# Performance work log

Measured on AMD Instinct MI355X. Metric: run time of the kernel, lower is better.

Reference implementation:

```python
import jax, jax.numpy as jnp
from jax import lax
import numpy as np

T, B, D, H = 512, 256, 128, 256
SHIFT = 0.0


def setup_inputs() -> dict:
    key = jax.random.key(0)
    ks = jax.random.split(key, 11)
    s_in = 1.0 / np.sqrt(D + H)
    s_cl = 1.0 / np.sqrt(H)
    return {
        "inputs": jax.random.normal(ks[0], (T, B, D), dtype=jnp.float32),
        "Wf": jax.random.normal(ks[1], (H, D + H), dtype=jnp.float32) * s_in,
        "bf": jax.random.normal(ks[2], (H,), dtype=jnp.float32) * s_in,
        "Wi": jax.random.normal(ks[3], (H, D + H), dtype=jnp.float32) * s_in,
        "bi": jax.random.normal(ks[4], (H,), dtype=jnp.float32) * s_in,
        "Wg": jax.random.normal(ks[5], (H, D + H), dtype=jnp.float32) * s_in,
        "bg": jax.random.normal(ks[6], (H,), dtype=jnp.float32) * s_in,
        "Wo": jax.random.normal(ks[7], (H, D + H), dtype=jnp.float32) * s_in,
        "bo": jax.random.normal(ks[8], (H,), dtype=jnp.float32) * s_in,
        "Wc": jax.random.normal(ks[9], (1, H), dtype=jnp.float32) * s_cl,
        "bc": jax.random.normal(ks[10], (1,), dtype=jnp.float32) * s_cl,
    }


def reference(inputs, Wf, bf, Wi, bi, Wg, bg, Wo, bo, Wc, bc):
    # Fuse the four gate linears into one GEMM per step: [4H, D+H]
    W = jnp.concatenate([Wf, Wi, Wg, Wo], axis=0)
    b = jnp.concatenate([bf, bi, bg, bo], axis=0)
    h = W.shape[0] // 4
    batch = inputs.shape[1]

    def step(carry, x):
        hx, cx = carry
        combined = jnp.concatenate([x, hx], axis=1)      # [B, D+H]
        z = combined @ W.T + b                            # [B, 4H]
        f = jax.nn.sigmoid(z[:, 0 * h:1 * h])
        i = jax.nn.sigmoid(z[:, 1 * h:2 * h])
        g = jnp.tanh(z[:, 2 * h:3 * h])
        o = jax.nn.sigmoid(z[:, 3 * h:4 * h])
        cx = f * cx + i * g
        hx = o * jnp.tanh(cx)
        return (hx, cx), hx

    h0 = jnp.zeros((batch, h), dtype=inputs.dtype)
    c0 = jnp.zeros((batch, h), dtype=inputs.dtype)
    (hx, cx), hs = lax.scan(step, (h0, c0), inputs)       # hs: [T, B, H]

    logits = hs @ Wc.T + bc                               # [T, B, 1]
    probs = jax.nn.sigmoid(logits + SHIFT)
    return (jnp.concatenate([probs, 1.0 - probs], axis=-1), hx, cx)
```

## Files before the change

kernel.cpp:

```cpp
#include <hip/hip_runtime.h>
#include <hip/hip_bf16.h>


#define T_STEPS 512
#define BATCH   256
#define DIN     128
#define HID     256
#define KDIM    384
#define LDK     392
#define GRIDN   256
#define NPOLL   96

typedef __attribute__((ext_vector_type(8))) short short8;
typedef __attribute__((ext_vector_type(4))) short short4v;
typedef __attribute__((ext_vector_type(4))) float f32x4;

__device__ __forceinline__ unsigned short f2bf(float f) {
    unsigned u = __float_as_uint(f);
    unsigned r = (u + 0x7FFFu + ((u >> 16) & 1u)) >> 16;
    return (unsigned short)r;
}
__device__ __forceinline__ float bf2f(unsigned short s) {
    return __uint_as_float(((unsigned)s) << 16);
}
__device__ __forceinline__ float sigmoid_f(float x) {
    return 1.f / (1.f + __expf(-x));
}
__device__ __forceinline__ float tanh_f(float x) {
    float e = __expf(2.f * x);
    return 1.f - 2.f / (e + 1.f);
}
__device__ __forceinline__ void poll_load_sc0(const unsigned int* p, uint4& a,
                                              uint4& b, uint4& c, uint4& d) {
    asm volatile(
        "global_load_dwordx4 %0, %4, off sc0\n\t"
        "global_load_dwordx4 %1, %4, off offset:16 sc0\n\t"
        "global_load_dwordx4 %2, %4, off offset:32 sc0\n\t"
        "global_load_dwordx4 %3, %4, off offset:48 sc0\n\t"
        "s_waitcnt vmcnt(0)"
        : "=&v"(a), "=&v"(b), "=&v"(c), "=&v"(d) : "v"(p) : "memory");
}
__device__ __forceinline__ void poll_load_sc1(const unsigned int* p, uint4& a,
                                              uint4& b, uint4& c, uint4& d) {
    asm volatile(
        "global_load_dwordx4 %0, %4, off sc1\n\t"
        "global_load_dwordx4 %1, %4, off offset:16 sc1\n\t"
        "global_load_dwordx4 %2, %4, off offset:32 sc1\n\t"
        "global_load_dwordx4 %3, %4, off offset:48 sc1\n\t"
        "s_waitcnt vmcnt(0)"
        : "=&v"(a), "=&v"(b), "=&v"(c), "=&v"(d) : "v"(p) : "memory");
}
__device__ __forceinline__ void store_plain_u32(unsigned int* p, unsigned int v) {
    asm volatile("global_store_dword %0, %1, off" :: "v"(p), "v"(v) : "memory");
}
__device__ __forceinline__ void store_sc1_u32(unsigned int* p, unsigned int v) {
    asm volatile("global_store_dword %0, %1, off sc1" :: "v"(p), "v"(v) : "memory");
}
__device__ __forceinline__ unsigned pack2bf(unsigned lo, unsigned hi) {
    return (hi & 0xFFFF0000u) | (lo >> 16);
}
__device__ __forceinline__ bool tags_ok(const uint4& a, const uint4& b,
                                        const uint4& c, const uint4& d,
                                        unsigned tag) {
    return ((a.x ^ tag) & 0xFFFFu) == 0 && ((a.y ^ tag) & 0xFFFFu) == 0 &&
           ((a.z ^ tag) & 0xFFFFu) == 0 && ((a.w ^ tag) & 0xFFFFu) == 0 &&
           ((b.x ^ tag) & 0xFFFFu) == 0 && ((b.y ^ tag) & 0xFFFFu) == 0 &&
           ((b.z ^ tag) & 0xFFFFu) == 0 && ((b.w ^ tag) & 0xFFFFu) == 0 &&
           ((c.x ^ tag) & 0xFFFFu) == 0 && ((c.y ^ tag) & 0xFFFFu) == 0 &&
           ((c.z ^ tag) & 0xFFFFu) == 0 && ((c.w ^ tag) & 0xFFFFu) == 0 &&
           ((d.x ^ tag) & 0xFFFFu) == 0 && ((d.y ^ tag) & 0xFFFFu) == 0 &&
           ((d.z ^ tag) & 0xFFFFu) == 0 && ((d.w ^ tag) & 0xFFFFu) == 0;
}

__global__ __launch_bounds__(256) void pack_w(
    const float* __restrict__ Wf, const float* __restrict__ Wi,
    const float* __restrict__ Wg, const float* __restrict__ Wo,
    unsigned short* __restrict__ Wp) {
    int idx = blockIdx.x * 256 + threadIdx.x;
    int n = idx / KDIM;
    int k = idx - n * KDIM;
    int g = n >> 8, j = n & 255;
    const float* s = (g == 0) ? Wf : (g == 1) ? Wi : (g == 2) ? Wg : Wo;
    Wp[idx] = f2bf(s[j * KDIM + k]);
}

__global__ __launch_bounds__(256) void pack_b(
    const float* __restrict__ bf, const float* __restrict__ bi,
    const float* __restrict__ bg, const float* __restrict__ bo,
    float* __restrict__ bp) {
    int n = blockIdx.x * 256 + threadIdx.x;
    int g = n >> 8, j = n & 255;
    const float* s = (g == 0) ? bf : (g == 1) ? bi : (g == 2) ? bg : bo;
    bp[n] = s[j];
}

__global__ __launch_bounds__(256) void init_k(unsigned int* __restrict__ hxp) {
    int tid = blockIdx.x * 256 + threadIdx.x;
    hxp[tid] = 0u;
    hxp[65536 + tid] = 0u;
    hxp[131072 + tid] = 0u;
    hxp[196608 + tid] = 0u;
}

__global__ __launch_bounds__(256, 1) void lstm_persist(
    const float* __restrict__ X,
    const unsigned short* __restrict__ W,
    const float* __restrict__ bias,
    unsigned int* __restrict__ hxp,
    unsigned short* __restrict__ hist,
    float* __restrict__ out) {
    __shared__ __align__(16) unsigned short W_s[64 * LDK];
    __shared__ __align__(16) unsigned short comb_s[16 * LDK];
    __shared__ __align__(16) float z_s[4 * 272];
    __shared__ int fastok_s;

    const int tid = threadIdx.x;
    const int bg = blockIdx.x & 15, jg = blockIdx.x >> 4;
    const int b0 = bg * 16, j0 = jg * 16;
    const int wave = tid >> 6, lane = tid & 63;
    const int l16 = lane & 15, quad = lane >> 4;
    const int bi = tid >> 4, jj = tid & 15;
    const int b = b0 + bi, j = j0 + jj;

#pragma unroll
    for (int c = 0; c < 12; ++c) {
        int q = c * 256 + tid;
        int row = q / 48, c8 = q - row * 48;
        int g = row >> 4, jr = row & 15;
        short8 v = *(const short8*)(W + ((g * 256 + j0 + jr) * KDIM + c8 * 8));
        *(short8*)(&W_s[row * LDK + c8 * 8]) = v;
    }
    const float bs0 = bias[0 * HID + j];
    const float bs1 = bias[1 * HID + j];
    const float bs2 = bias[2 * HID + j];
    const float bs3 = bias[3 * HID + j];
    if (tid == 0) fastok_s = 1;

    float c_reg = 0.f;
    float h_final = 0.f;

    const unsigned short* arow = &comb_s[l16 * LDK + quad * 8];
    const unsigned short* brow = &W_s[(wave * 16 + l16) * LDK + quad * 8];
    const int hrow = tid >> 4, hc = tid & 15;
    const int xr0 = tid >> 5, xc4 = tid & 31, xr1 = (tid + 256) >> 5;

    const float* xb = X + b0 * DIN;
    float4 xv0 = *(const float4*)(xb + xr0 * DIN + xc4 * 4);
    float4 xv1 = *(const float4*)(xb + xr1 * DIN + xc4 * 4);

    __syncthreads();

    for (int k = 0; k < T_STEPS; ++k) {
        const unsigned tag = (unsigned)k;
        const unsigned int* fb =
            hxp + (k & 1) * 65536 + (b0 + hrow) * HID + hc * 16;
        const unsigned int* sb = fb + 131072;
        uint4 a, bq, cq, d;
        const int usefast = fastok_s;

        {
            short4v r;
            r.x = (short)f2bf(xv0.x); r.y = (short)f2bf(xv0.y);
            r.z = (short)f2bf(xv0.z); r.w = (short)f2bf(xv0.w);
            *(short4v*)(&comb_s[xr0 * LDK + xc4 * 4]) = r;
            r.x = (short)f2bf(xv1.x); r.y = (short)f2bf(xv1.y);
            r.z = (short)f2bf(xv1.z); r.w = (short)f2bf(xv1.w);
            *(short4v*)(&comb_s[xr1 * LDK + xc4 * 4]) = r;
        }

        if (usefast) {
            int tries = NPOLL;
            bool ok = false;
            for (;;) {
                poll_load_sc0(fb, a, bq, cq, d);
                if (tags_ok(a, bq, cq, d, tag)) { ok = true; break; }
                if (--tries == 0) break;
            }
            if (!ok) {
                fastok_s = 0;
                for (;;) {
                    poll_load_sc1(sb, a, bq, cq, d);
                    if (tags_ok(a, bq, cq, d, tag)) break;
                    __builtin_amdgcn_s_sleep(1);
                }
            }
        } else {
            for (;;) {
                poll_load_sc1(sb, a, bq, cq, d);
                if (tags_ok(a, bq, cq, d, tag)) break;
                __builtin_amdgcn_s_sleep(1);
            }
        }

        {
            uint4 p0, p1;
            p0.x = pack2bf(a.x, a.y);   p0.y = pack2bf(a.z, a.w);
            p0.z = pack2bf(bq.x, bq.y); p0.w = pack2bf(bq.z, bq.w);
            p1.x = pack2bf(cq.x, cq.y); p1.y = pack2bf(cq.z, cq.w);
            p1.z = pack2bf(d.x, d.y);   p1.w = pack2bf(d.z, d.w);
            *(uint4*)(&comb_s[hrow * LDK + DIN + hc * 16]) = p0;
            *(uint4*)(&comb_s[hrow * LDK + DIN + hc * 16 + 8]) = p1;
        }
        __syncthreads();

        f32x4 acc0 = {0.f, 0.f, 0.f, 0.f}, acc1 = {0.f, 0.f, 0.f, 0.f};
#pragma unroll
        for (int kt = 0; kt < 6; ++kt) {
            short8 a0 = *(const short8*)(arow + (2 * kt) * 32);
            short8 b0v = *(const short8*)(brow + (2 * kt) * 32);
            short8 a1 = *(const short8*)(arow + (2 * kt + 1) * 32);
            short8 b1v = *(const short8*)(brow + (2 * kt + 1) * 32);
            acc0 = __builtin_amdgcn_mfma_f32_16x16x32_bf16(a0, b0v, acc0, 0, 0, 0);
            acc1 = __builtin_amdgcn_mfma_f32_16x16x32_bf16(a1, b1v, acc1, 0, 0, 0);
        }
#pragma unroll
        for (int r = 0; r < 4; ++r)
            z_s[wave * 272 + (quad * 4 + r) * 17 + l16] = acc0[r] + acc1[r];
        __syncthreads();

        float zf = z_s[0 * 272 + bi * 17 + jj] + bs0;
        float zi = z_s[1 * 272 + bi * 17 + jj] + bs1;
        float zg = z_s[2 * 272 + bi * 17 + jj] + bs2;
        float zo = z_s[3 * 272 + bi * 17 + jj] + bs3;
        float fg = sigmoid_f(zf);
        float ig = sigmoid_f(zi);
        float gg = tanh_f(zg);
        float og = sigmoid_f(zo);
        c_reg = fg * c_reg + ig * gg;
        float hval = og * tanh_f(c_reg);
        unsigned short hb = f2bf(hval);
        unsigned int hword = ((unsigned)hb << 16) | (unsigned)(k + 1);
        unsigned int* fdst = hxp + ((k + 1) & 1) * 65536 + b * HID + j;
        store_plain_u32(fdst, hword);
        store_sc1_u32(fdst + 131072, hword);
        hist[(size_t)k * BATCH * HID + b * HID + j] = hb;
        if (k + 1 < T_STEPS) {
            const float* xn = X + (size_t)(k + 1) * BATCH * DIN + b0 * DIN;
            xv0 = *(const float4*)(xn + xr0 * DIN + xc4 * 4);
            xv1 = *(const float4*)(xn + xr1 * DIN + xc4 * 4);
        } else {
            h_final = hval;
        }
    }

    out[T_STEPS * BATCH * 2 + b * HID + j] = h_final;
    out[T_STEPS * BATCH * 2 + BATCH * HID + b * HID + j] = c_reg;
}

__global__ __launch_bounds__(256) void probs_k(
    const unsigned short* __restrict__ hist, const float* __restrict__ Wc,
    const float* __restrict__ bc, float* __restrict__ out) {
    const int wave = threadIdx.x >> 6, lane = threadIdx.x & 63;
    const size_t row = (size_t)blockIdx.x * 4 + wave;
    const unsigned short* h = hist + row * HID;
    short4v hv = *(const short4v*)(h + lane * 4);
    const float4 wv = *(const float4*)(Wc + lane * 4);
    float p = bf2f((unsigned short)hv.x) * wv.x + bf2f((unsigned short)hv.y) * wv.y +
              bf2f((unsigned short)hv.z) * wv.z + bf2f((unsigned short)hv.w) * wv.w;
#pragma unroll
    for (int off = 32; off >= 1; off >>= 1) p += __shfl_down(p, off);
    if (lane == 0) {
        float prob = 1.f / (1.f + __expf(-(p + bc[0])));
        out[row * 2]     = prob;
        out[row * 2 + 1] = 1.f - prob;
    }
}

extern "C" void kernel_launch(void* const* d_in, const int* in_sizes, int n_in,
                              void* d_out, int out_size, void* d_ws, size_t ws_size,
                              hipStream_t stream) {
    const float* X  = (const float*)d_in[0];
    const float* Wf = (const float*)d_in[1];
    const float* bfp= (const float*)d_in[2];
    const float* Wi = (const float*)d_in[3];
    const float* bip= (const float*)d_in[4];
    const float* Wg = (const float*)d_in[5];
    const float* bgp= (const float*)d_in[6];
    const float* Wo = (const float*)d_in[7];
    const float* bop= (const float*)d_in[8];
    const float* Wc = (const float*)d_in[9];
    const float* bc = (const float*)d_in[10];
    float* out = (float*)d_out;

    char* ws = (char*)d_ws;
    unsigned short* Wpack = (unsigned short*)(ws);
    float* bias = (float*)(ws + 786432);
    unsigned int* hxp = (unsigned int*)(ws + 790528);
    unsigned short* hist = (unsigned short*)(ws + 1839104);

    pack_w<<<1536, 256, 0, stream>>>(Wf, Wi, Wg, Wo, Wpack);
    pack_b<<<4, 256, 0, stream>>>(bfp, bip, bgp, bop, bias);
    init_k<<<256, 256, 0, stream>>>(hxp);

    void* kargs[6] = {(void*)&X, (void*)&Wpack, (void*)&bias,
                      (void*)&hxp, (void*)&hist, (void*)&out};
    (void)hipLaunchCooperativeKernel((const void*)lstm_persist, dim3(GRIDN),
                                     dim3(256), kargs, 0, stream);

    probs_k<<<32768, 256, 0, stream>>>(hist, Wc, bc, out);
}
```

Baseline: 1.189 ms.

## Halve persistent grid, widen blocks, precompute input projection off the critical path

The persistent LSTM kernel now runs 128 blocks of 512 threads, each covering 32 hidden units instead of 16. Fewer blocks take part in the per-step cross-block handoff, and each thread polls only two 16-byte chunks. The x-part of the gate GEMM (the first two K-tiles) for step k+1 is computed after step k's update, so only the h-part stays on the dependent chain. In exchange there is an extra __syncthreads per step, a short sleep inside the fast poll loop, and a doubled weight tile in LDS that may reduce occupancy headroom.

```diff
diff --git a/kernel.cpp b/kernel.cpp
--- a/kernel.cpp
+++ b/kernel.cpp
@@ -8,7 +8,8 @@
 #define HID     256
 #define KDIM    384
 #define LDK     392
-#define GRIDN   256
+#define GRIDN   128
+#define BLOCKT  512
 #define NPOLL   96
 
 typedef __attribute__((ext_vector_type(8))) short short8;
@@ -30,25 +31,21 @@
     float e = __expf(2.f * x);
     return 1.f - 2.f / (e + 1.f);
 }
-__device__ __forceinline__ void poll_load_sc0(const unsigned int* p, uint4& a,
-                                              uint4& b, uint4& c, uint4& d) {
+__device__ __forceinline__ void poll_load2_sc0(const unsigned int* p, uint4& a,
+                                               uint4& b) {
     asm volatile(
-        "global_load_dwordx4 %0, %4, off sc0\n\t"
-        "global_load_dwordx4 %1, %4, off offset:16 sc0\n\t"
-        "global_load_dwordx4 %2, %4, off offset:32 sc0\n\t"
-        "global_load_dwordx4 %3, %4, off offset:48 sc0\n\t"
+        "global_load_dwordx4 %0, %2, off sc0\n\t"
+        "global_load_dwordx4 %1, %2, off offset:16 sc0\n\t"
         "s_waitcnt vmcnt(0)"
-        : "=&v"(a), "=&v"(b), "=&v"(c), "=&v"(d) : "v"(p) : "memory");
-}
-__device__ __forceinline__ void poll_load_sc1(const unsigned int* p, uint4& a,
-                                              uint4& b, uint4& c, uint4& d) {
+        : "=&v"(a), "=&v"(b) : "v"(p) : "memory");
+}
+__device__ __forceinline__ void poll_load2_sc1(const unsigned int* p, uint4& a,
+                                               uint4& b) {
     asm volatile(
-        "global_load_dwordx4 %0, %4, off sc1\n\t"
-        "global_load_dwordx4 %1, %4, off offset:16 sc1\n\t"
-        "global_load_dwordx4 %2, %4, off offset:32 sc1\n\t"
-        "global_load_dwordx4 %3, %4, off offset:48 sc1\n\t"
+        "global_load_dwordx4 %0, %2, off sc1\n\t"
+        "global_load_dwordx4 %1, %2, off offset:16 sc1\n\t"
         "s_waitcnt vmcnt(0)"
-        : "=&v"(a), "=&v"(b), "=&v"(c), "=&v"(d) : "v"(p) : "memory");
+        : "=&v"(a), "=&v"(b) : "v"(p) : "memory");
 }
 __device__ __forceinline__ void store_plain_u32(unsigned int* p, unsigned int v) {
     asm volatile("global_store_dword %0, %1, off" :: "v"(p), "v"(v) : "memory");
@@ -59,17 +56,12 @@
 __device__ __forceinline__ unsigned pack2bf(unsigned lo, unsigned hi) {
     return (hi & 0xFFFF0000u) | (lo >> 16);
 }
-__device__ __forceinline__ bool tags_ok(const uint4& a, const uint4& b,
-                                        const uint4& c, const uint4& d,
-                                        unsigned tag) {
+__device__ __forceinline__ bool tags_ok2(const uint4& a, const uint4& b,
+                                         unsigned tag) {
     return ((a.x ^ tag) & 0xFFFFu) == 0 && ((a.y ^ tag) & 0xFFFFu) == 0 &&
            ((a.z ^ tag) & 0xFFFFu) == 0 && ((a.w ^ tag) & 0xFFFFu) == 0 &&
            ((b.x ^ tag) & 0xFFFFu) == 0 && ((b.y ^ tag) & 0xFFFFu) == 0 &&
-           ((b.z ^ tag) & 0xFFFFu) == 0 && ((b.w ^ tag) & 0xFFFFu) == 0 &&
-           ((c.x ^ tag) & 0xFFFFu) == 0 && ((c.y ^ tag) & 0xFFFFu) == 0 &&
-           ((c.z ^ tag) & 0xFFFFu) == 0 && ((c.w ^ tag) & 0xFFFFu) == 0 &&
-           ((d.x ^ tag) & 0xFFFFu) == 0 && ((d.y ^ tag) & 0xFFFFu) == 0 &&
-           ((d.z ^ tag) & 0xFFFFu) == 0 && ((d.w ^ tag) & 0xFFFFu) == 0;
+           ((b.z ^ tag) & 0xFFFFu) == 0 && ((b.w ^ tag) & 0xFFFFu) == 0;
 }
 
 __global__ __launch_bounds__(256) void pack_w(
@@ -102,31 +94,31 @@
     hxp[196608 + tid] = 0u;
 }
 
-__global__ __launch_bounds__(256, 1) void lstm_persist(
+__global__ __launch_bounds__(BLOCKT, 1) void lstm_persist(
     const float* __restrict__ X,
     const unsigned short* __restrict__ W,
     const float* __restrict__ bias,
     unsigned int* __restrict__ hxp,
     unsigned short* __restrict__ hist,
     float* __restrict__ out) {
-    __shared__ __align__(16) unsigned short W_s[64 * LDK];
+    __shared__ __align__(16) unsigned short W_s[128 * LDK];
     __shared__ __align__(16) unsigned short comb_s[16 * LDK];
-    __shared__ __align__(16) float z_s[4 * 272];
+    __shared__ __align__(16) float z_s[8 * 272];
     __shared__ int fastok_s;
 
     const int tid = threadIdx.x;
     const int bg = blockIdx.x & 15, jg = blockIdx.x >> 4;
-    const int b0 = bg * 16, j0 = jg * 16;
+    const int b0 = bg * 16, j0 = jg * 32;
     const int wave = tid >> 6, lane = tid & 63;
     const int l16 = lane & 15, quad = lane >> 4;
-    const int bi = tid >> 4, jj = tid & 15;
+    const int bi = tid >> 5, jj = tid & 31;
     const int b = b0 + bi, j = j0 + jj;
 
 #pragma unroll
     for (int c = 0; c < 12; ++c) {
-        int q = c * 256 + tid;
+        int q = c * 512 + tid;
         int row = q / 48, c8 = q - row * 48;
-        int g = row >> 4, jr = row & 15;
+        int g = row >> 5, jr = row & 31;
         short8 v = *(const short8*)(W + ((g * 256 + j0 + jr) * KDIM + c8 * 8));
         *(short8*)(&W_s[row * LDK + c8 * 8]) = v;
     }
@@ -141,71 +133,72 @@
 
     const unsigned short* arow = &comb_s[l16 * LDK + quad * 8];
     const unsigned short* brow = &W_s[(wave * 16 + l16) * LDK + quad * 8];
-    const int hrow = tid >> 4, hc = tid & 15;
-    const int xr0 = tid >> 5, xc4 = tid & 31, xr1 = (tid + 256) >> 5;
-
-    const float* xb = X + b0 * DIN;
-    float4 xv0 = *(const float4*)(xb + xr0 * DIN + xc4 * 4);
-    float4 xv1 = *(const float4*)(xb + xr1 * DIN + xc4 * 4);
-
+
+    float4 xv = *(const float4*)(X + b * DIN + jj * 4);
+    {
+        short4v r;
+        r.x = (short)f2bf(xv.x); r.y = (short)f2bf(xv.y);
+        r.z = (short)f2bf(xv.z); r.w = (short)f2bf(xv.w);
+        *(short4v*)(&comb_s[bi * LDK + jj * 4]) = r;
+    }
+    xv = *(const float4*)(X + (size_t)1 * BATCH * DIN + b * DIN + jj * 4);
     __syncthreads();
+
+    f32x4 acc_x0 = {0.f, 0.f, 0.f, 0.f}, acc_x1 = {0.f, 0.f, 0.f, 0.f};
+#pragma unroll
+    for (int kt = 0; kt < 2; ++kt) {
+        short8 a0 = *(const short8*)(arow + (2 * kt) * 32);
+        short8 b0v = *(const short8*)(brow + (2 * kt) * 32);
+        short8 a1 = *(const short8*)(arow + (2 * kt + 1) * 32);
+        short8 b1v = *(const short8*)(brow + (2 * kt + 1) * 32);
+        acc_x0 = __builtin_amdgcn_mfma_f32_16x16x32_bf16(a0, b0v, acc_x0, 0, 0, 0);
+        acc_x1 = __builtin_amdgcn_mfma_f32_16x16x32_bf16(a1, b1v, acc_x1, 0, 0, 0);
+    }
 
     for (int k = 0; k < T_STEPS; ++k) {
         const unsigned tag = (unsigned)k;
         const unsigned int* fb =
-            hxp + (k & 1) * 65536 + (b0 + hrow) * HID + hc * 16;
+            hxp + (k & 1) * 65536 + (b0 + bi) * HID + jj * 8;
         const unsigned int* sb = fb + 131072;
-        uint4 a, bq, cq, d;
+        uint4 a, bq;
         const int usefast = fastok_s;
-
-        {
-            short4v r;
-            r.x = (short)f2bf(xv0.x); r.y = (short)f2bf(xv0.y);
-            r.z = (short)f2bf(xv0.z); r.w = (short)f2bf(xv0.w);
-            *(short4v*)(&comb_s[xr0 * LDK + xc4 * 4]) = r;
-            r.x = (short)f2bf(xv1.x); r.y = (short)f2bf(xv1.y);
-            r.z = (short)f2bf(xv1.z); r.w = (short)f2bf(xv1.w);
-            *(short4v*)(&comb_s[xr1 * LDK + xc4 * 4]) = r;
-        }
 
         if (usefast) {
             int tries = NPOLL;
             bool ok = false;
             for (;;) {
-                poll_load_sc0(fb, a, bq, cq, d);
-                if (tags_ok(a, bq, cq, d, tag)) { ok = true; break; }
+                poll_load2_sc0(fb, a, bq);
+                if (tags_ok2(a, bq, tag)) { ok = true; break; }
                 if (--tries == 0) break;
+                __builtin_amdgcn_s_sleep(1);
             }
             if (!ok) {
                 fastok_s = 0;
                 for (;;) {
-                    poll_load_sc1(sb, a, bq, cq, d);
-                    if (tags_ok(a, bq, cq, d, tag)) break;
+                    poll_load2_sc1(sb, a, bq);
+                    if (tags_ok2(a, bq, tag)) break;
                     __builtin_amdgcn_s_sleep(1);
                 }
             }
         } else {
             for (;;) {
-                poll_load_sc1(sb, a, bq, cq, d);
-                if (tags_ok(a, bq, cq, d, tag)) break;
+                poll_load2_sc1(sb, a, bq);
+                if (tags_ok2(a, bq, tag)) break;
                 __builtin_amdgcn_s_sleep(1);
             }
         }
 
         {
-            uint4 p0, p1;
+            uint4 p0;
             p0.x = pack2bf(a.x, a.y);   p0.y = pack2bf(a.z, a.w);
             p0.z = pack2bf(bq.x, bq.y); p0.w = pack2bf(bq.z, bq.w);
-            p1.x = pack2bf(cq.x, cq.y); p1.y = pack2bf(cq.z, cq.w);
-            p1.z = pack2bf(d.x, d.y);   p1.w = pack2bf(d.z, d.w);
-            *(uint4*)(&comb_s[hrow * LDK + DIN + hc * 16]) = p0;
-            *(uint4*)(&comb_s[hrow * LDK + DIN + hc * 16 + 8]) = p1;
+            *(uint4*)(&comb_s[bi * LDK + DIN + jj * 8]) = p0;
         }
         __syncthreads();
 
-        f32x4 acc0 = {0.f, 0.f, 0.f, 0.f}, acc1 = {0.f, 0.f, 0.f, 0.f};
-#pragma unroll
-        for (int kt = 0; kt < 6; ++kt) {
+        f32x4 acc0 = acc_x0, acc1 = acc_x1;
+#pragma unroll
+        for (int kt = 2; kt < 6; ++kt) {
             short8 a0 = *(const short8*)(arow + (2 * kt) * 32);
             short8 b0v = *(const short8*)(brow + (2 * kt) * 32);
             short8 a1 = *(const short8*)(arow + (2 * kt + 1) * 32);
@@ -218,10 +211,12 @@
             z_s[wave * 272 + (quad * 4 + r) * 17 + l16] = acc0[r] + acc1[r];
         __syncthreads();
 
-        float zf = z_s[0 * 272 + bi * 17 + jj] + bs0;
-        float zi = z_s[1 * 272 + bi * 17 + jj] + bs1;
-        float zg = z_s[2 * 272 + bi * 17 + jj] + bs2;
-        float zo = z_s[3 * 272 + bi * 17 + jj] + bs3;
+        const int zc = bi * 17 + (jj & 15);
+        const int zw = (jj >> 4) * 272;
+        float zf = z_s[zw + 0 * 544 + zc] + bs0;
+        float zi = z_s[zw + 1 * 544 + zc] + bs1;
+        float zg = z_s[zw + 2 * 544 + zc] + bs2;
+        float zo = z_s[zw + 3 * 544 + zc] + bs3;
         float fg = sigmoid_f(zf);
         float ig = sigmoid_f(zi);
         float gg = tanh_f(zg);
@@ -234,12 +229,33 @@
         store_plain_u32(fdst, hword);
         store_sc1_u32(fdst + 131072, hword);
         hist[(size_t)k * BATCH * HID + b * HID + j] = hb;
+
         if (k + 1 < T_STEPS) {
-            const float* xn = X + (size_t)(k + 1) * BATCH * DIN + b0 * DIN;
-            xv0 = *(const float4*)(xn + xr0 * DIN + xc4 * 4);
-            xv1 = *(const float4*)(xn + xr1 * DIN + xc4 * 4);
+            short4v r;
+            r.x = (short)f2bf(xv.x); r.y = (short)f2bf(xv.y);
+            r.z = (short)f2bf(xv.z); r.w = (short)f2bf(xv.w);
+            *(short4v*)(&comb_s[bi * LDK + jj * 4]) = r;
+            if (k + 2 < T_STEPS) {
+                xv = *(const float4*)(X + (size_t)(k + 2) * BATCH * DIN +
+                                      b * DIN + jj * 4);
+            }
         } else {
             h_final = hval;
+        }
+        __syncthreads();
+
+        if (k + 1 < T_STEPS) {
+            f32x4 ax0 = {0.f, 0.f, 0.f, 0.f}, ax1 = {0.f, 0.f, 0.f, 0.f};
+#pragma unroll
+            for (int kt = 0; kt < 2; ++kt) {
+                short8 a0 = *(const short8*)(arow + (2 * kt) * 32);
+                short8 b0v = *(const short8*)(brow + (2 * kt) * 32);
+                short8 a1 = *(const short8*)(arow + (2 * kt + 1) * 32);
+                short8 b1v = *(const short8*)(brow + (2 * kt + 1) * 32);
+                ax0 = __builtin_amdgcn_mfma_f32_16x16x32_bf16(a0, b0v, ax0, 0, 0, 0);
+                ax1 = __builtin_amdgcn_mfma_f32_16x16x32_bf16(a1, b1v, ax1, 0, 0, 0);
+            }
+            acc_x0 = ax0; acc_x1 = ax1;
         }
     }
 
@@ -295,7 +311,7 @@
     void* kargs[6] = {(void*)&X, (void*)&Wpack, (void*)&bias,
                       (void*)&hxp, (void*)&hist, (void*)&out};
     (void)hipLaunchCooperativeKernel((const void*)lstm_persist, dim3(GRIDN),
-                                     dim3(256), kargs, 0, stream);
+                                     dim3(BLOCKT), kargs, 0, stream);
 
     probs_k<<<32768, 256, 0, stream>>>(hist, Wc, bc, out);
 }
```

Result: slower. 1.295 ms (+8.9%).

## Assign block roles by XCD so each batch group stays on one chiplet

Applied to the files above, without the earlier changes.

Each persistent block reads its XCD id from a hardware register and claims a role slot on that XCD. Roles are mapped so the 16 blocks sharing a batch group (bg = role>>4) sit on the same XCD, and overflow blocks take any unclaimed role after a grid sync. The aim is to keep the per-step hidden-state exchange inside one XCD's L2, cutting cross-chiplet coherence traffic. The cost is a cooperative grid sync at startup, and the launch must be cooperative for cg::this_grid().sync() to be valid.

```diff
diff --git a/kernel.cpp b/kernel.cpp
--- a/kernel.cpp
+++ b/kernel.cpp
@@ -1,5 +1,8 @@
 #include <hip/hip_runtime.h>
 #include <hip/hip_bf16.h>
+#include <hip/hip_cooperative_groups.h>
+
+namespace cg = cooperative_groups;
 
 
 #define T_STEPS 512
@@ -14,6 +17,9 @@
 typedef __attribute__((ext_vector_type(8))) short short8;
 typedef __attribute__((ext_vector_type(4))) short short4v;
 typedef __attribute__((ext_vector_type(4))) float f32x4;
+
+__device__ unsigned boot_percxd[8];
+__device__ unsigned boot_claimed[8];
 
 __device__ __forceinline__ unsigned short f2bf(float f) {
     unsigned u = __float_as_uint(f);
@@ -100,6 +106,10 @@
     hxp[65536 + tid] = 0u;
     hxp[131072 + tid] = 0u;
     hxp[196608 + tid] = 0u;
+    if (tid < 8) {
+        boot_percxd[tid] = 0u;
+        boot_claimed[tid] = 0u;
+    }
 }
 
 __global__ __launch_bounds__(256, 1) void lstm_persist(
@@ -113,9 +123,37 @@
     __shared__ __align__(16) unsigned short comb_s[16 * LDK];
     __shared__ __align__(16) float z_s[4 * 272];
     __shared__ int fastok_s;
+    __shared__ int role_s;
 
     const int tid = threadIdx.x;
-    const int bg = blockIdx.x & 15, jg = blockIdx.x >> 4;
+
+    if (tid == 0) {
+        unsigned xcc = __builtin_amdgcn_s_getreg((31u << 11) | 20u) & 7u;
+        unsigned slot = atomicAdd(&boot_percxd[xcc], 1u);
+        int role = -1;
+        if (slot < 32u) {
+            role = (int)(xcc * 32u + slot);
+            atomicOr(&boot_claimed[role >> 5], 1u << (role & 31));
+        }
+        role_s = role;
+        fastok_s = 1;
+    }
+    __syncthreads();
+    cg::this_grid().sync();
+    if (role_s < 0) {
+        if (tid == 0) {
+            for (int r = 0; r < 256; ++r) {
+                unsigned bit = 1u << (r & 31);
+                if (!(atomicOr(&boot_claimed[r >> 5], bit) & bit)) {
+                    role_s = r;
+                    break;
+                }
+            }
+        }
+        __syncthreads();
+    }
+    const int role = role_s;
+    const int bg = role >> 4, jg = role & 15;
     const int b0 = bg * 16, j0 = jg * 16;
     const int wave = tid >> 6, lane = tid & 63;
     const int l16 = lane & 15, quad = lane >> 4;
@@ -134,7 +172,6 @@
     const float bs1 = bias[1 * HID + j];
     const float bs2 = bias[2 * HID + j];
     const float bs3 = bias[3 * HID + j];
-    if (tid == 0) fastok_s = 1;
 
     float c_reg = 0.f;
     float h_final = 0.f;
```

Measured after the change: 1.203 ms. Within noise of the previous version (+1.2%).

## Interleave gate weights, keep W in registers, use shuffles instead of LDS

Applied to the files above, without the earlier changes.

Packs the weights and biases gate-interleaved (row = 4*j + gate), so each wave's MFMA output tile holds all four gates for its (b, j) pairs. A 4-lane transpose with xor shuffles then delivers f, i, g, o to one lane. This removes the z_s shared buffer and one __syncthreads per step. The weight tile also moves from LDS into 12 registers per lane, which removes B-operand LDS reads. The combined buffer is double-buffered and the next step's x load is issued right after the barrier, cutting per-step latency on the serial recurrence at the cost of more registers.

```diff
diff --git a/kernel.cpp b/kernel.cpp
--- a/kernel.cpp
+++ b/kernel.cpp
@@ -79,7 +79,7 @@
     int idx = blockIdx.x * 256 + threadIdx.x;
     int n = idx / KDIM;
     int k = idx - n * KDIM;
-    int g = n >> 8, j = n & 255;
+    int j = n >> 2, g = n & 3;
     const float* s = (g == 0) ? Wf : (g == 1) ? Wi : (g == 2) ? Wg : Wo;
     Wp[idx] = f2bf(s[j * KDIM + k]);
 }
@@ -89,7 +89,7 @@
     const float* __restrict__ bg, const float* __restrict__ bo,
     float* __restrict__ bp) {
     int n = blockIdx.x * 256 + threadIdx.x;
-    int g = n >> 8, j = n & 255;
+    int j = n >> 2, g = n & 3;
     const float* s = (g == 0) ? bf : (g == 1) ? bi : (g == 2) ? bg : bo;
     bp[n] = s[j];
 }
@@ -109,9 +109,7 @@
     unsigned int* __restrict__ hxp,
     unsigned short* __restrict__ hist,
     float* __restrict__ out) {
-    __shared__ __align__(16) unsigned short W_s[64 * LDK];
-    __shared__ __align__(16) unsigned short comb_s[16 * LDK];
-    __shared__ __align__(16) float z_s[4 * 272];
+    __shared__ __align__(16) unsigned short comb_s[2 * 16 * LDK];
     __shared__ int fastok_s;
 
     const int tid = threadIdx.x;
@@ -119,54 +117,49 @@
     const int b0 = bg * 16, j0 = jg * 16;
     const int wave = tid >> 6, lane = tid & 63;
     const int l16 = lane & 15, quad = lane >> 4;
-    const int bi = tid >> 4, jj = tid & 15;
-    const int b = b0 + bi, j = j0 + jj;
-
+    const int hrow = tid >> 4, hc = tid & 15;
+    const int xr0 = tid >> 5, xc4 = tid & 31, xr1 = (tid + 256) >> 5;
+
+    const int b = b0 + quad * 4 + (l16 & 3);
+    const int j = j0 + (wave << 2) + (l16 >> 2);
+
+    const unsigned short* wrow =
+        W + (size_t)(4 * (j0 + (wave << 2)) + l16) * KDIM + quad * 8;
+    short8 wb[12];
 #pragma unroll
-    for (int c = 0; c < 12; ++c) {
-        int q = c * 256 + tid;
-        int row = q / 48, c8 = q - row * 48;
-        int g = row >> 4, jr = row & 15;
-        short8 v = *(const short8*)(W + ((g * 256 + j0 + jr) * KDIM + c8 * 8));
-        *(short8*)(&W_s[row * LDK + c8 * 8]) = v;
-    }
-    const float bs0 = bias[0 * HID + j];
-    const float bs1 = bias[1 * HID + j];
-    const float bs2 = bias[2 * HID + j];
-    const float bs3 = bias[3 * HID + j];
+    for (int kt = 0; kt < 12; ++kt) wb[kt] = *(const short8*)(wrow + kt * 32);
+
+    const float4 bb = *(const float4*)(bias + j * 4);
     if (tid == 0) fastok_s = 1;
 
     float c_reg = 0.f;
     float h_final = 0.f;
 
-    const unsigned short* arow = &comb_s[l16 * LDK + quad * 8];
-    const unsigned short* brow = &W_s[(wave * 16 + l16) * LDK + quad * 8];
-    const int hrow = tid >> 4, hc = tid & 15;
-    const int xr0 = tid >> 5, xc4 = tid & 31, xr1 = (tid + 256) >> 5;
-
-    const float* xb = X + b0 * DIN;
-    float4 xv0 = *(const float4*)(xb + xr0 * DIN + xc4 * 4);
-    float4 xv1 = *(const float4*)(xb + xr1 * DIN + xc4 * 4);
-
+    {
+        const float* x0b = X + b0 * DIN;
+        float4 t0 = *(const float4*)(x0b + xr0 * DIN + xc4 * 4);
+        float4 t1 = *(const float4*)(x0b + xr1 * DIN + xc4 * 4);
+        short4v r;
+        r.x = (short)f2bf(t0.x); r.y = (short)f2bf(t0.y);
+        r.z = (short)f2bf(t0.z); r.w = (short)f2bf(t0.w);
+        *(short4v*)(&comb_s[xr0 * LDK + xc4 * 4]) = r;
+        r.x = (short)f2bf(t1.x); r.y = (short)f2bf(t1.y);
+        r.z = (short)f2bf(t1.z); r.w = (short)f2bf(t1.w);
+        *(short4v*)(&comb_s[xr1 * LDK + xc4 * 4]) = r;
+    }
+    float4 xv0 = *(const float4*)(X + (size_t)BATCH * DIN + b0 * DIN + xr0 * DIN + xc4 * 4);
+    float4 xv1 = *(const float4*)(X + (size_t)BATCH * DIN + b0 * DIN + xr1 * DIN + xc4 * 4);
     __syncthreads();
 
     for (int k = 0; k < T_STEPS; ++k) {
+        const int p = k & 1;
+        unsigned short* cbuf = &comb_s[p * 16 * LDK];
         const unsigned tag = (unsigned)k;
         const unsigned int* fb =
             hxp + (k & 1) * 65536 + (b0 + hrow) * HID + hc * 16;
         const unsigned int* sb = fb + 131072;
         uint4 a, bq, cq, d;
         const int usefast = fastok_s;
-
-        {
-            short4v r;
-            r.x = (short)f2bf(xv0.x); r.y = (short)f2bf(xv0.y);
-            r.z = (short)f2bf(xv0.z); r.w = (short)f2bf(xv0.w);
-            *(short4v*)(&comb_s[xr0 * LDK + xc4 * 4]) = r;
-            r.x = (short)f2bf(xv1.x); r.y = (short)f2bf(xv1.y);
-            r.z = (short)f2bf(xv1.z); r.w = (short)f2bf(xv1.w);
-            *(short4v*)(&comb_s[xr1 * LDK + xc4 * 4]) = r;
-        }
 
         if (usefast) {
             int tries = NPOLL;
@@ -198,34 +191,54 @@
             p0.z = pack2bf(bq.x, bq.y); p0.w = pack2bf(bq.z, bq.w);
             p1.x = pack2bf(cq.x, cq.y); p1.y = pack2bf(cq.z, cq.w);
             p1.z = pack2bf(d.x, d.y);   p1.w = pack2bf(d.z, d.w);
-            *(uint4*)(&comb_s[hrow * LDK + DIN + hc * 16]) = p0;
-            *(uint4*)(&comb_s[hrow * LDK + DIN + hc * 16 + 8]) = p1;
+            *(uint4*)(&cbuf[hrow * LDK + DIN + hc * 16]) = p0;
+            *(uint4*)(&cbuf[hrow * LDK + DIN + hc * 16 + 8]) = p1;
+        }
+        if (k > 0) {
+            short4v r;
+            r.x = (short)f2bf(xv0.x); r.y = (short)f2bf(xv0.y);
+            r.z = (short)f2bf(xv0.z); r.w = (short)f2bf(xv0.w);
+            *(short4v*)(&cbuf[xr0 * LDK + xc4 * 4]) = r;
+            r.x = (short)f2bf(xv1.x); r.y = (short)f2bf(xv1.y);
+            r.z = (short)f2bf(xv1.z); r.w = (short)f2bf(xv1.w);
+            *(short4v*)(&cbuf[xr1 * LDK + xc4 * 4]) = r;
         }
         __syncthreads();
 
+        if (k + 1 < T_STEPS) {
+            const float* xn = X + (size_t)(k + 1) * BATCH * DIN + b0 * DIN;
+            xv0 = *(const float4*)(xn + xr0 * DIN + xc4 * 4);
+            xv1 = *(const float4*)(xn + xr1 * DIN + xc4 * 4);
+        }
         f32x4 acc0 = {0.f, 0.f, 0.f, 0.f}, acc1 = {0.f, 0.f, 0.f, 0.f};
+        const unsigned short* ap = &cbuf[l16 * LDK + quad * 8];
 #pragma unroll
         for (int kt = 0; kt < 6; ++kt) {
-            short8 a0 = *(const short8*)(arow + (2 * kt) * 32);
-            short8 b0v = *(const short8*)(brow + (2 * kt) * 32);
-            short8 a1 = *(const short8*)(arow + (2 * kt + 1) * 32);
-            short8 b1v = *(const short8*)(brow + (2 * kt + 1) * 32);
-            acc0 = __builtin_amdgcn_mfma_f32_16x16x32_bf16(a0, b0v, acc0, 0, 0, 0);
-            acc1 = __builtin_amdgcn_mfma_f32_16x16x32_bf16(a1, b1v, acc1, 0, 0, 0);
-        }
-#pragma unroll
-        for (int r = 0; r < 4; ++r)
-            z_s[wave * 272 + (quad * 4 + r) * 17 + l16] = acc0[r] + acc1[r];
-        __syncthreads();
-
-        float zf = z_s[0 * 272 + bi * 17 + jj] + bs0;
-        float zi = z_s[1 * 272 + bi * 17 + jj] + bs1;
-        float zg = z_s[2 * 272 + bi * 17 + jj] + bs2;
-        float zo = z_s[3 * 272 + bi * 17 + jj] + bs3;
-        float fg = sigmoid_f(zf);
-        float ig = sigmoid_f(zi);
-        float gg = tanh_f(zg);
-        float og = sigmoid_f(zo);
+            short8 a0 = *(const short8*)(ap + (2 * kt) * 32);
+            short8 a1 = *(const short8*)(ap + (2 * kt + 1) * 32);
+            acc0 = __builtin_amdgcn_mfma_f32_16x16x32_bf16(a0, wb[2 * kt], acc0, 0, 0, 0);
+            acc1 = __builtin_amdgcn_mfma_f32_16x16x32_bf16(a1, wb[2 * kt + 1], acc1, 0, 0, 0);
+        }
+
+        float v0 = acc0[0] + acc1[0];
+        float v1 = acc0[1] + acc1[1];
+        float v2 = acc0[2] + acc1[2];
+        float v3 = acc0[3] + acc1[3];
+        const bool o1 = (lane & 1), o2 = (lane & 2);
+        float t, u;
+        t = o1 ? v0 : v1; u = __shfl_xor(t, 1);
+        v1 = o1 ? v1 : u; v0 = o1 ? u : v0;
+        t = o1 ? v2 : v3; u = __shfl_xor(t, 1);
+        v3 = o1 ? v3 : u; v2 = o1 ? u : v2;
+        t = o2 ? v0 : v2; u = __shfl_xor(t, 2);
+        v2 = o2 ? v2 : u; v0 = o2 ? u : v0;
+        t = o2 ? v1 : v3; u = __shfl_xor(t, 2);
+        v3 = o2 ? v3 : u; v1 = o2 ? u : v1;
+
+        float fg = sigmoid_f(v0 + bb.x);
+        float ig = sigmoid_f(v1 + bb.y);
+        float gg = tanh_f(v2 + bb.z);
+        float og = sigmoid_f(v3 + bb.w);
         c_reg = fg * c_reg + ig * gg;
         float hval = og * tanh_f(c_reg);
         unsigned short hb = f2bf(hval);
@@ -234,13 +247,7 @@
         store_plain_u32(fdst, hword);
         store_sc1_u32(fdst + 131072, hword);
         hist[(size_t)k * BATCH * HID + b * HID + j] = hb;
-        if (k + 1 < T_STEPS) {
-            const float* xn = X + (size_t)(k + 1) * BATCH * DIN + b0 * DIN;
-            xv0 = *(const float4*)(xn + xr0 * DIN + xc4 * 4);
-            xv1 = *(const float4*)(xn + xr1 * DIN + xc4 * 4);
-        } else {
-            h_final = hval;
-        }
+        if (k + 1 == T_STEPS) h_final = hval;
     }
 
     out[T_STEPS * BATCH * 2 + b * HID + j] = h_final;
```

Result: slower. 3.091 ms (+159.9%).
